# Optimization experiments

Hardware: AMD Instinct MI355X
Metric: run time of the kernel (lower is better)

The kernel has to match this reference:

```python
import jax, jax.numpy as jnp
import numpy as np

N = 50000
E = 800000
F_IN = 128


def _gat(h, src, dst, W, a_src, a_dst, bias, heads, out_ch, concat):
    n = h.shape[0]
    z = (h @ W.T).reshape(n, heads, out_ch)              # [N,H,C]
    alpha_s = jnp.sum(z * a_src, axis=-1)                # [N,H]
    alpha_d = jnp.sum(z * a_dst, axis=-1)                # [N,H]
    logits = jax.nn.leaky_relu(alpha_s[src] + alpha_d[dst], 0.2)  # [Etot,H]
    m = jax.ops.segment_max(logits, dst, num_segments=n)
    ex = jnp.exp(logits - m[dst])
    denom = jax.ops.segment_sum(ex, dst, num_segments=n)
    w = ex / (denom[dst] + 1e-16)                        # [Etot,H]
    agg = jax.ops.segment_sum(w[:, :, None] * z[src], dst, num_segments=n)  # [N,H,C]
    if concat:
        out = agg.reshape(n, heads * out_ch)
    else:
        out = agg.mean(axis=1)
    return out + bias


def setup_inputs() -> dict:
    key = jax.random.key(0)
    ks = jax.random.split(key, 16)
    s = lambda *sh: 1.0 / np.sqrt(sh[-1])
    inp = {
        "x": jax.random.normal(ks[0], (N, F_IN), jnp.float32),
        "edge_index": jax.random.randint(ks[1], (2, E), 0, N, jnp.int64),
        # GraphConv(no_node_features=128 -> 128, aggr='add')
        "W_rel": jax.random.normal(ks[2], (128, F_IN), jnp.float32) * s(128, F_IN),
        "b_rel": jnp.zeros((128,), jnp.float32),
        "W_root": jax.random.normal(ks[3], (128, F_IN), jnp.float32) * s(128, F_IN),
        # GATConv(128 -> 8, heads=8, concat) => 64
        "W1": jax.random.normal(ks[4], (64, 128), jnp.float32) * s(64, 128),
        "a1_src": jax.random.normal(ks[5], (8, 8), jnp.float32) * 0.35,
        "a1_dst": jax.random.normal(ks[6], (8, 8), jnp.float32) * 0.35,
        "b1": jnp.zeros((64,), jnp.float32),
        # GATConv(64 -> 64, heads=1, concat=False)
        "W2": jax.random.normal(ks[7], (64, 64), jnp.float32) * s(64, 64),
        "a2_src": jax.random.normal(ks[8], (1, 64), jnp.float32) * 0.125,
        "a2_dst": jax.random.normal(ks[9], (1, 64), jnp.float32) * 0.125,
        "b2": jnp.zeros((64,), jnp.float32),
        "Wr": jax.random.normal(ks[10], (1, 64), jnp.float32) * s(1, 64),
        "br": jnp.zeros((1,), jnp.float32),
    }
    return inp


def reference(x, edge_index, W_rel, b_rel, W_root, W1, a1_src, a1_dst, b1,
              W2, a2_src, a2_dst, b2, Wr, br):
    src, dst = edge_index[0], edge_index[1]
    # GraphConv, aggr='add': W_rel @ sum_{j in N(i)} x_j + b + W_root @ x_i
    nbr = jax.ops.segment_sum(x[src], dst, num_segments=N)
    h = nbr @ W_rel.T + b_rel + x @ W_root.T
    h = jax.nn.elu(h)
    # GATConv adds self-loops by default
    loop = jnp.arange(N, dtype=edge_index.dtype)
    src2 = jnp.concatenate([src, loop])
    dst2 = jnp.concatenate([dst, loop])
    h = _gat(h, src2, dst2, W1, a1_src, a1_dst, b1, heads=8, out_ch=8, concat=True)
    h = jax.nn.elu(h)
    h = _gat(h, src2, dst2, W2, a2_src, a2_dst, b2, heads=1, out_ch=64, concat=False)
    # final 'mean' aggregation over all nodes (single graph)
    g = jnp.mean(h, axis=0, keepdims=True)               # [1,64]
    return g @ Wr.T + br                                  # [1,1]
```

## Files before the change

kernel.cpp:

```cpp
#include <hip/hip_runtime.h>
#include <hip/hip_bf16.h>
#include <math.h>

#define N_NODES 50000
#define N_EDGES 800000
#define F_IN 128
#define NBUCK 391
#define EPB 4096
#define NBB 196

typedef __attribute__((ext_vector_type(8))) short bf16x8;
typedef __attribute__((ext_vector_type(4))) float f32x4;
typedef __attribute__((ext_vector_type(2))) float f32x2;
typedef unsigned long long ull;

__device__ __forceinline__ float elu_f(float x)   { return x > 0.f ? x : expm1f(x); }
__device__ __forceinline__ float lrelu_f(float x) { return x > 0.f ? x : 0.2f * x; }
__device__ __forceinline__ int   clampN(int v)    { return v < 0 ? 0 : (v >= N_NODES ? N_NODES - 1 : v); }
__device__ __forceinline__ float bits2f(unsigned int u) { union { unsigned int u; float f; } x; x.u = u; return x.f; }
__device__ __forceinline__ float bf2f(unsigned short s) { return bits2f(((unsigned int)s) << 16); }
__device__ __forceinline__ unsigned short f2bfbits(float f) {
    __hip_bfloat16 b = __float2bfloat16(f);
    return __builtin_bit_cast(unsigned short, b);
}
__device__ __forceinline__ unsigned int pack2(float lo, float hi) {
    return ((unsigned int)f2bfbits(hi) << 16) | f2bfbits(lo);
}

#define CAST_X_IDS (N_NODES * 32)
#define CAST_IDS (CAST_X_IDS + 32768 + 8192 + 4096)
#define CASTB ((CAST_IDS + 255) / 256)
__global__ __launch_bounds__(256) void k_prep(const int* __restrict__ dst,
                                              const float* __restrict__ x,
                                              const float* __restrict__ W_rel,
                                              const float* __restrict__ W_root,
                                              const float* __restrict__ W1,
                                              const float* __restrict__ W2,
                                              int* __restrict__ part,
                                              __hip_bfloat16* __restrict__ Abuf,
                                              unsigned int* __restrict__ x8,
                                              __hip_bfloat16* __restrict__ Wc,
                                              __hip_bfloat16* __restrict__ W1b,
                                              __hip_bfloat16* __restrict__ W2b,
                                              float* __restrict__ red) {
    __shared__ int hist[NBUCK];
    int tid = threadIdx.x;
    if (blockIdx.x < NBB) {
        for (int j = tid; j < NBUCK; j += 256) hist[j] = 0;
        __syncthreads();
        int base = blockIdx.x * EPB;
        #pragma unroll
        for (int t = 0; t < EPB / 256; ++t) {
            int e = base + t * 256 + tid;
            if (e < N_EDGES) atomicAdd(&hist[clampN(dst[e]) >> 7], 1);
        }
        __syncthreads();
        for (int j = tid; j < NBUCK; j += 256)
            part[(size_t)blockIdx.x * NBUCK + j] = hist[j];
    } else {
        if (blockIdx.x == NBB) red[tid] = 0.f;
        int id = (blockIdx.x - NBB) * 256 + tid;
        if (id < CAST_X_IDS) {
            int i = id >> 5, c4 = (id & 31) * 4;
            float4 v = *(const float4*)&x[(size_t)i * 128 + c4];
            ull p = (ull)f2bfbits(v.x) | ((ull)f2bfbits(v.y) << 16)
                  | ((ull)f2bfbits(v.z) << 32) | ((ull)f2bfbits(v.w) << 48);
            *(ull*)&Abuf[(size_t)i * 256 + 128 + c4] = p;
            int t = __builtin_amdgcn_cvt_pk_fp8_f32(v.x, v.y, 0, false);
            t = __builtin_amdgcn_cvt_pk_fp8_f32(v.z, v.w, t, true);
            x8[(size_t)i * 32 + (id & 31)] = (unsigned int)t;
        } else if (id < CAST_IDS) {
            int j = id - CAST_X_IDS;
            if (j < 32768) {
                int cc = j >> 8, k = j & 255;
                float v = (k < 128) ? W_rel[cc * 128 + k] : W_root[cc * 128 + (k - 128)];
                Wc[j] = __float2bfloat16(v);
            } else if (j < 32768 + 8192) {
                W1b[j - 32768] = __float2bfloat16(W1[j - 32768]);
            } else {
                W2b[j - 32768 - 8192] = __float2bfloat16(W2[j - 32768 - 8192]);
            }
        }
    }
}

__global__ __launch_bounds__(512) void k_bscan(const int* __restrict__ part,
                                               int* __restrict__ boff,
                                               int* __restrict__ bcur) {
    __shared__ int wsum[8];
    __shared__ int wbase[8];
    int tid = threadIdx.x;
    int lane = tid & 63, wid = tid >> 6;
    int v = 0;
    if (tid < NBUCK) {
        for (int b = 0; b < NBB; ++b) v += part[(size_t)b * NBUCK + tid];
    }
    int x = v;
    #pragma unroll
    for (int d = 1; d < 64; d <<= 1) {
        int t = __shfl_up(x, d, 64);
        if (lane >= d) x += t;
    }
    if (lane == 63) wsum[wid] = x;
    __syncthreads();
    if (tid == 0) {
        int b = 0;
        #pragma unroll
        for (int w = 0; w < 8; ++w) { wbase[w] = b; b += wsum[w]; }
    }
    __syncthreads();
    if (tid < NBUCK) {
        int e = wbase[wid] + x - v;
        boff[tid] = e;
        bcur[tid] = e;
    }
    if (tid == 0) boff[NBUCK] = N_EDGES;
}

__global__ __launch_bounds__(256) void k_bscatter(const int* __restrict__ src,
                                                  const int* __restrict__ dst,
                                                  int* __restrict__ bcur,
                                                  unsigned int* __restrict__ ebuf) {
    __shared__ int hist[NBUCK];
    __shared__ int hbase[NBUCK];
    int tid = threadIdx.x;
    for (int j = tid; j < NBUCK; j += 256) hist[j] = 0;
    __syncthreads();
    int base = blockIdx.x * EPB;
    unsigned int myP[EPB / 256]; int myB[EPB / 256], myR[EPB / 256];
    #pragma unroll
    for (int t = 0; t < EPB / 256; ++t) {
        int e = base + t * 256 + tid;
        if (e < N_EDGES) {
            int d = clampN(dst[e]);
            int s = clampN(src[e]);
            myP[t] = ((unsigned int)s << 7) | (unsigned int)(d & 127);
            myB[t] = d >> 7;
            myR[t] = atomicAdd(&hist[d >> 7], 1);
        } else myB[t] = -1;
    }
    __syncthreads();
    for (int j = tid; j < NBUCK; j += 256)
        if (hist[j]) hbase[j] = atomicAdd(&bcur[j], hist[j]);
    __syncthreads();
    #pragma unroll
    for (int t = 0; t < EPB / 256; ++t) {
        if (myB[t] >= 0) ebuf[hbase[myB[t]] + myR[t]] = myP[t];
    }
}

__global__ __launch_bounds__(256) void k_bfinal(const unsigned int* __restrict__ ebuf,
                                                const int* __restrict__ boff,
                                                int* __restrict__ offsets,
                                                int* __restrict__ csr) {
    __shared__ int cnt[128];
    __shared__ int cur[128];
    __shared__ int ws[4];
    int b = blockIdx.x;
    int tid = threadIdx.x;
    int node0 = b << 7;
    int k0 = boff[b], k1 = boff[b + 1];
    if (tid < 128) cnt[tid] = 0;
    __syncthreads();
    for (int k = k0 + tid; k < k1; k += 256)
        atomicAdd(&cnt[ebuf[k] & 127u], 1);
    __syncthreads();
    int lane = tid & 63;
    int v = (tid < 128) ? cnt[tid] : 0;
    int x = v;
    #pragma unroll
    for (int d = 1; d < 64; d <<= 1) {
        int t = __shfl_up(x, d, 64);
        if (lane >= d) x += t;
    }
    if (lane == 63) ws[tid >> 6] = x;
    __syncthreads();
    if (tid < 128) {
        int add = (tid >> 6) ? ws[0] : 0;
        int excl = k0 + add + x - v;
        cur[tid] = excl;
        int node = node0 + tid;
        if (node < N_NODES) offsets[node] = excl;
    }
    if (b == NBUCK - 1 && tid == 0) offsets[N_NODES] = N_EDGES;
    __syncthreads();
    for (int k = k0 + tid; k < k1; k += 256) {
        unsigned int e = ebuf[k];
        int r = atomicAdd(&cur[e & 127u], 1);
        csr[r] = (int)(e >> 7);
    }
}

__global__ __launch_bounds__(256) void k_gather(const unsigned int* __restrict__ x8,
                                                const int* __restrict__ offsets,
                                                const int* __restrict__ csr,
                                                ull* __restrict__ outNbr) {
    int i = blockIdx.x * 8 + (threadIdx.x >> 5);
    int l = threadIdx.x & 31;
    int k0 = offsets[i], k1 = offsets[i + 1];
    float a0 = 0.f, a1 = 0.f, a2 = 0.f, a3 = 0.f;
    for (int kb = k0; kb < k1; kb += 8) {
        int s[8]; int vm[8];
        #pragma unroll
        for (int j = 0; j < 8; ++j) {
            int kk = kb + j;
            vm[j] = kk < k1;
            s[j] = csr[vm[j] ? kk : k1 - 1];
        }
        unsigned int u[8];
        #pragma unroll
        for (int j = 0; j < 8; ++j) u[j] = x8[(size_t)s[j] * 32 + l];
        #pragma unroll
        for (int j = 0; j < 8; ++j) {
            if (vm[j]) {
                f32x2 lo = __builtin_amdgcn_cvt_pk_f32_fp8(u[j], false);
                f32x2 hi = __builtin_amdgcn_cvt_pk_f32_fp8(u[j], true);
                a0 += lo.x; a1 += lo.y; a2 += hi.x; a3 += hi.y;
            }
        }
    }
    outNbr[(size_t)i * 64 + l] = (ull)pack2(a0, a1) | ((ull)pack2(a2, a3) << 32);
}

__global__ __launch_bounds__(256) void k_gemm12(const __hip_bfloat16* __restrict__ A,
                                                const __hip_bfloat16* __restrict__ Wc,
                                                const float* __restrict__ bias,
                                                const __hip_bfloat16* __restrict__ W1b,
                                                const float* __restrict__ a_src,
                                                const float* __restrict__ a_dst,
                                                float* __restrict__ as_o,
                                                float* __restrict__ ad_o,
                                                unsigned int* __restrict__ z8) {
    __shared__ __align__(16) short smem[64 * 136];
    short (*sA)[40] = (short(*)[40])smem;
    short (*sW)[40] = (short(*)[40])(smem + 64 * 40);
    int tid = threadIdx.x;
    int lane = tid & 63, wave = tid >> 6;
    int quad = lane >> 4, l16 = lane & 15;
    int node0 = blockIdx.x * 64;
    int srow = tid >> 2, schk = (tid & 3) * 8;
    int ga = node0 + srow; if (ga >= N_NODES) ga = N_NODES - 1;
    const short* Ap = (const short*)A + (size_t)ga * 256 + schk;
    const short* Wp = (const short*)Wc;
    f32x4 acc[8];
    #pragma unroll
    for (int t = 0; t < 8; ++t) acc[t] = (f32x4){0.f, 0.f, 0.f, 0.f};
    for (int k0 = 0; k0 < 256; k0 += 32) {
        *(bf16x8*)&sA[srow][schk] = *(const bf16x8*)(Ap + k0);
        #pragma unroll
        for (int it = 0; it < 2; ++it) {
            int wrow = srow + it * 64;
            *(bf16x8*)&sW[wrow][schk] = *(const bf16x8*)(Wp + (size_t)wrow * 256 + k0 + schk);
        }
        __syncthreads();
        bf16x8 a = *(const bf16x8*)&sA[wave * 16 + l16][quad * 8];
        #pragma unroll
        for (int nt = 0; nt < 8; ++nt) {
            bf16x8 b = *(const bf16x8*)&sW[nt * 16 + l16][quad * 8];
            acc[nt] = __builtin_amdgcn_mfma_f32_16x16x32_bf16(a, b, acc[nt], 0, 0, 0);
        }
        __syncthreads();
    }
    #pragma unroll
    for (int nt = 0; nt < 8; ++nt) {
        int col = nt * 16 + l16;
        float bv = bias[col];
        #pragma unroll
        for (int r = 0; r < 4; ++r) {
            int row = wave * 16 + quad * 4 + r;
            smem[row * 136 + col] = (short)f2bfbits(elu_f(acc[nt][r] + bv));
        }
    }
    __syncthreads();
    f32x4 acc2[4];
    #pragma unroll
    for (int t = 0; t < 4; ++t) acc2[t] = (f32x4){0.f, 0.f, 0.f, 0.f};
    const short* W1p = (const short*)W1b;
    #pragma unroll
    for (int k0 = 0; k0 < 128; k0 += 32) {
        bf16x8 a = *(const bf16x8*)&smem[(wave * 16 + l16) * 136 + k0 + quad * 8];
        #pragma unroll
        for (int nt = 0; nt < 4; ++nt) {
            bf16x8 b = *(const bf16x8*)(W1p + (size_t)(nt * 16 + l16) * 128 + k0 + quad * 8);
            acc2[nt] = __builtin_amdgcn_mfma_f32_16x16x32_bf16(a, b, acc2[nt], 0, 0, 0);
        }
    }
    __syncthreads();
    #pragma unroll
    for (int nt = 0; nt < 4; ++nt) {
        int col = nt * 16 + l16;
        #pragma unroll
        for (int r = 0; r < 4; ++r) {
            int row = wave * 16 + quad * 4 + r;
            smem[row * 72 + col] = (short)f2bfbits(acc2[nt][r]);
        }
    }
    __syncthreads();
    int row = tid >> 2, chunk = tid & 3;
    int gi = node0 + row;
    float v[16];
    bf16x8 c0 = *(const bf16x8*)&smem[row * 72 + chunk * 16];
    bf16x8 c1 = *(const bf16x8*)&smem[row * 72 + chunk * 16 + 8];
    #pragma unroll
    for (int j = 0; j < 8; ++j) {
        v[j]     = bf2f((unsigned short)c0[j]);
        v[8 + j] = bf2f((unsigned short)c1[j]);
    }
    float ps0 = 0.f, pd0 = 0.f, ps1 = 0.f, pd1 = 0.f;
    #pragma unroll
    for (int j = 0; j < 8; ++j) {
        ps0 += v[j] * a_src[chunk * 16 + j];
        pd0 += v[j] * a_dst[chunk * 16 + j];
        ps1 += v[8 + j] * a_src[chunk * 16 + 8 + j];
        pd1 += v[8 + j] * a_dst[chunk * 16 + 8 + j];
    }
    if (gi < N_NODES) {
        as_o[(size_t)gi * 8 + 2 * chunk]     = ps0;
        as_o[(size_t)gi * 8 + 2 * chunk + 1] = ps1;
        ad_o[(size_t)gi * 8 + 2 * chunk]     = pd0;
        ad_o[(size_t)gi * 8 + 2 * chunk + 1] = pd1;
        #pragma unroll
        for (int wi = 0; wi < 4; ++wi) {
            int t = __builtin_amdgcn_cvt_pk_fp8_f32(v[4 * wi], v[4 * wi + 1], 0, false);
            t = __builtin_amdgcn_cvt_pk_fp8_f32(v[4 * wi + 2], v[4 * wi + 3], t, true);
            z8[(size_t)gi * 16 + chunk * 4 + wi] = (unsigned int)t;
        }
    }
}

__global__ __launch_bounds__(256) void k_gat1z2(const unsigned int* __restrict__ z8,
                                                const float* __restrict__ as1,
                                                const float* __restrict__ ad1,
                                                const float* __restrict__ b1,
                                                const int* __restrict__ offsets,
                                                const int* __restrict__ csr,
                                                const __hip_bfloat16* __restrict__ W2b,
                                                const float* __restrict__ a2s,
                                                const float* __restrict__ a2d,
                                                float* __restrict__ as2,
                                                float* __restrict__ ad2,
                                                unsigned int* __restrict__ z2e8) {
    __shared__ __align__(16) short sH2[16 * 72];
    __shared__ __align__(16) short sZ2[16 * 72];
    int iloc = threadIdx.x >> 4;
    int i = blockIdx.x * 16 + iloc;
    int l = threadIdx.x & 15;
    int hd = l >> 1;
    int wh = l & 7, slot = l >> 3;
    int k0 = offsets[i], k1 = offsets[i + 1];
    float ad_h = ad1[(size_t)i * 8 + hd];
    float adw  = ad1[(size_t)i * 8 + wh];
    float e_self = __expf(lrelu_f(as1[(size_t)i * 8 + hd] + ad_h));
    unsigned int uz = z8[(size_t)i * 16 + l];
    f32x2 zlo = __builtin_amdgcn_cvt_pk_f32_fp8(uz, false);
    f32x2 zhi = __builtin_amdgcn_cvt_pk_f32_fp8(uz, true);
    float acc0 = e_self * zlo.x, acc1 = e_self * zlo.y;
    float acc2 = e_self * zhi.x, acc3 = e_self * zhi.y;
    float denp = 0.f;
    for (int kb = k0; kb < k1; kb += 8) {
        int sr[4]; float er[4];
        #pragma unroll
        for (int m = 0; m < 4; ++m) {
            int kk = kb + 2 * m + slot;
            bool v = kk < k1;
            int s = csr[v ? kk : k1 - 1];
            sr[m] = s;
            er[m] = v ? __expf(lrelu_f(as1[(size_t)s * 8 + wh] + adw)) : 0.f;
            denp += er[m];
        }
        int sj[8]; float ej[8]; unsigned int u[8];
        #pragma unroll
        for (int m = 0; m < 4; ++m) {
            #pragma unroll
            for (int sb = 0; sb < 2; ++sb) {
                sj[2 * m + sb] = __shfl(sr[m], sb * 8 + hd, 16);
                ej[2 * m + sb] = __shfl(er[m], sb * 8 + hd, 16);
            }
        }
        #pragma unroll
        for (int j = 0; j < 8; ++j) u[j] = z8[(size_t)sj[j] * 16 + l];
        #pragma unroll
        for (int j = 0; j < 8; ++j) {
            f32x2 alo = __builtin_amdgcn_cvt_pk_f32_fp8(u[j], false);
            f32x2 ahi = __builtin_amdgcn_cvt_pk_f32_fp8(u[j], true);
            acc0 += ej[j] * alo.x; acc1 += ej[j] * alo.y;
            acc2 += ej[j] * ahi.x; acc3 += ej[j] * ahi.y;
        }
    }
    denp += __shfl_xor(denp, 8, 16);
    float den = __shfl(denp, hd, 16) + e_self;
    float inv = 1.f / den;
    float r0 = elu_f(acc0 * inv + b1[4 * l + 0]);
    float r1 = elu_f(acc1 * inv + b1[4 * l + 1]);
    float r2 = elu_f(acc2 * inv + b1[4 * l + 2]);
    float r3 = elu_f(acc3 * inv + b1[4 * l + 3]);
    *(ull*)&sH2[iloc * 72 + 4 * l] = (ull)pack2(r0, r1) | ((ull)pack2(r2, r3) << 32);
    __syncthreads();
    int lane = threadIdx.x & 63, wave = threadIdx.x >> 6;
    int quad = lane >> 4, l16 = lane & 15;
    f32x4 accz = (f32x4){0.f, 0.f, 0.f, 0.f};
    const short* W2p = (const short*)W2b;
    #pragma unroll
    for (int kk0 = 0; kk0 < 64; kk0 += 32) {
        bf16x8 a = *(const bf16x8*)&sH2[l16 * 72 + kk0 + quad * 8];
        bf16x8 b = *(const bf16x8*)(W2p + (size_t)(wave * 16 + l16) * 64 + kk0 + quad * 8);
        accz = __builtin_amdgcn_mfma_f32_16x16x32_bf16(a, b, accz, 0, 0, 0);
    }
    #pragma unroll
    for (int r = 0; r < 4; ++r)
        sZ2[(quad * 4 + r) * 72 + wave * 16 + l16] = (short)f2bfbits(accz[r]);
    __syncthreads();
    ull pz = *(const ull*)&sZ2[iloc * 72 + 4 * l];
    float v0 = bf2f((unsigned short)(pz & 0xffff));
    float v1 = bf2f((unsigned short)((pz >> 16) & 0xffff));
    float v2 = bf2f((unsigned short)((pz >> 32) & 0xffff));
    float v3 = bf2f((unsigned short)(pz >> 48));
    float ps = v0 * a2s[4 * l + 0] + v1 * a2s[4 * l + 1] + v2 * a2s[4 * l + 2] + v3 * a2s[4 * l + 3];
    float pd = v0 * a2d[4 * l + 0] + v1 * a2d[4 * l + 1] + v2 * a2d[4 * l + 2] + v3 * a2d[4 * l + 3];
    #pragma unroll
    for (int d = 8; d >= 1; d >>= 1) {
        ps += __shfl_xor(ps, d, 16);
        pd += __shfl_xor(pd, d, 16);
    }
    if (l == 0) { as2[i] = ps; ad2[i] = pd; }
    int t = __builtin_amdgcn_cvt_pk_fp8_f32(v0, v1, 0, false);
    t = __builtin_amdgcn_cvt_pk_fp8_f32(v2, v3, t, true);
    z2e8[(size_t)i * 16 + l] = (unsigned int)t;
}

__global__ __launch_bounds__(256) void k_gat2attn(const unsigned int* __restrict__ z8,
                                                  const float* __restrict__ as2,
                                                  const float* __restrict__ ad2,
                                                  const float* __restrict__ b2,
                                                  const int* __restrict__ offsets,
                                                  const int* __restrict__ csr,
                                                  const float* __restrict__ Wr,
                                                  float* __restrict__ red) {
    int i = blockIdx.x * 16 + (threadIdx.x >> 4);
    int l = threadIdx.x & 15;
    int k0 = offsets[i], k1 = offsets[i + 1];
    float ad = ad2[i];
    float e_self = __expf(lrelu_f(as2[i] + ad));
    unsigned int uz = z8[(size_t)i * 16 + l];
    f32x2 zlo = __builtin_amdgcn_cvt_pk_f32_fp8(uz, false);
    f32x2 zhi = __builtin_amdgcn_cvt_pk_f32_fp8(uz, true);
    float acc0 = e_self * zlo.x, acc1 = e_self * zlo.y;
    float acc2 = e_self * zhi.x, acc3 = e_self * zhi.y;
    float denp = (l == 0) ? e_self : 0.f;
    for (int kb = k0; kb < k1; kb += 16) {
        int kk = kb + l;
        bool v = kk < k1;
        int s = csr[v ? kk : k1 - 1];
        float e = v ? __expf(lrelu_f(as2[s] + ad)) : 0.f;
        denp += e;
        int nv = k1 - kb; if (nv > 16) nv = 16;
        for (int j0 = 0; j0 < nv; j0 += 8) {
            int sj[8]; float ej[8]; unsigned int u[8];
            #pragma unroll
            for (int j = 0; j < 8; ++j) {
                int idx = (j0 + j) & 15;
                sj[j] = __shfl(s, idx, 16);
                ej[j] = __shfl(e, idx, 16);
            }
            #pragma unroll
            for (int j = 0; j < 8; ++j) u[j] = z8[(size_t)sj[j] * 16 + l];
            #pragma unroll
            for (int j = 0; j < 8; ++j) {
                f32x2 alo = __builtin_amdgcn_cvt_pk_f32_fp8(u[j], false);
                f32x2 ahi = __builtin_amdgcn_cvt_pk_f32_fp8(u[j], true);
                acc0 += ej[j] * alo.x; acc1 += ej[j] * alo.y;
                acc2 += ej[j] * ahi.x; acc3 += ej[j] * ahi.y;
            }
        }
    }
    #pragma unroll
    for (int d = 8; d >= 1; d >>= 1) denp += __shfl_xor(denp, d, 16);
    float inv = 1.f / denp;
    float c = (acc0 * inv + b2[4 * l + 0]) * Wr[4 * l + 0]
            + (acc1 * inv + b2[4 * l + 1]) * Wr[4 * l + 1]
            + (acc2 * inv + b2[4 * l + 2]) * Wr[4 * l + 2]
            + (acc3 * inv + b2[4 * l + 3]) * Wr[4 * l + 3];
    #pragma unroll
    for (int d = 8; d >= 1; d >>= 1) c += __shfl_xor(c, d, 64);
    if (l == 0) atomicAdd(&red[blockIdx.x & 255], c);
}

__global__ void k_finalize(const float* __restrict__ red, const float* __restrict__ br,
                           float* __restrict__ out) {
    int t = threadIdx.x;
    float s = red[t] + red[t + 64] + red[t + 128] + red[t + 192];
    #pragma unroll
    for (int d = 32; d >= 1; d >>= 1) s += __shfl_xor(s, d, 64);
    if (t == 0) out[0] = s * (1.0f / N_NODES) + br[0];
}

extern "C" void kernel_launch(void* const* d_in, const int* in_sizes, int n_in,
                              void* d_out, int out_size, void* d_ws, size_t ws_size,
                              hipStream_t stream) {
    const float* x      = (const float*)d_in[0];
    const int*   edges  = (const int*)d_in[1];
    const float* W_rel  = (const float*)d_in[2];
    const float* b_rel  = (const float*)d_in[3];
    const float* W_root = (const float*)d_in[4];
    const float* W1     = (const float*)d_in[5];
    const float* a1s    = (const float*)d_in[6];
    const float* a1d    = (const float*)d_in[7];
    const float* b1     = (const float*)d_in[8];
    const float* W2     = (const float*)d_in[9];
    const float* a2s    = (const float*)d_in[10];
    const float* a2d    = (const float*)d_in[11];
    const float* b2     = (const float*)d_in[12];
    const float* Wr     = (const float*)d_in[13];
    const float* br     = (const float*)d_in[14];
    float* out = (float*)d_out;

    const int* src = edges;
    const int* dst = edges + N_EDGES;

    char* ws = (char*)d_ws;
    size_t p = 0;
    auto alloc = [&](size_t bytes) -> void* {
        void* r = ws + p;
        p = (p + bytes + 255) & ~(size_t)255;
        return r;
    };
    int*   part    = (int*)alloc((size_t)NBB * NBUCK * 4);
    int*   boff    = (int*)alloc((size_t)(NBUCK + 1) * 4);
    int*   bcur    = (int*)alloc((size_t)NBUCK * 4);
    unsigned int* ebuf = (unsigned int*)alloc((size_t)N_EDGES * 4);
    int*   offsets = (int*)alloc((size_t)(N_NODES + 1) * 4);
    int*   csr     = (int*)alloc((size_t)N_EDGES * 4);
    __hip_bfloat16* Abuf = (__hip_bfloat16*)alloc((size_t)N_NODES * 256 * 2);
    unsigned int* x8 = (unsigned int*)alloc((size_t)N_NODES * 32 * 4);
    __hip_bfloat16* Wc   = (__hip_bfloat16*)alloc((size_t)128 * 256 * 2);
    __hip_bfloat16* W1b  = (__hip_bfloat16*)alloc((size_t)64 * 128 * 2);
    __hip_bfloat16* W2b  = (__hip_bfloat16*)alloc((size_t)64 * 64 * 2);
    float* as1 = (float*)alloc((size_t)N_NODES * 8 * 4);
    float* ad1 = (float*)alloc((size_t)N_NODES * 8 * 4);
    float* as2 = (float*)alloc((size_t)N_NODES * 4);
    float* ad2 = (float*)alloc((size_t)N_NODES * 4);
    unsigned int* z1e8 = (unsigned int*)alloc((size_t)N_NODES * 16 * 4);
    unsigned int* z2e8 = (unsigned int*)alloc((size_t)N_NODES * 16 * 4);
    float* red = (float*)alloc(256 * 4);

    const int MB   = (N_NODES + 63) / 64;
    const int NB8  = N_NODES / 8;
    const int NB16 = N_NODES / 16;

    k_prep    <<<NBB + CASTB, 256, 0, stream>>>(dst, x, W_rel, W_root, W1, W2,
                                                part, Abuf, x8, Wc, W1b, W2b, red);
    k_bscan   <<<1, 512, 0, stream>>>(part, boff, bcur);
    k_bscatter<<<NBB, 256, 0, stream>>>(src, dst, bcur, ebuf);
    k_bfinal  <<<NBUCK, 256, 0, stream>>>(ebuf, boff, offsets, csr);
    k_gather  <<<NB8, 256, 0, stream>>>(x8, offsets, csr, (ull*)Abuf);
    k_gemm12  <<<MB, 256, 0, stream>>>(Abuf, Wc, b_rel, W1b, a1s, a1d, as1, ad1, z1e8);
    k_gat1z2  <<<NB16, 256, 0, stream>>>(z1e8, as1, ad1, b1, offsets, csr,
                                         W2b, a2s, a2d, as2, ad2, z2e8);
    k_gat2attn<<<NB16, 256, 0, stream>>>(z2e8, as2, ad2, b2, offsets, csr, Wr, red);
    k_finalize<<<1, 64, 0, stream>>>(red, br, out);
}
```

Baseline: 241.6 us.

## Fuse post-prep pipeline into one cooperative persistent kernel with grid syncs

Replaces eight separate kernel launches (bucket scan, scatter, CSR finalize, gather, GEMM, GAT1+Z2, GAT2 attention, finalize) with one cooperative kernel that loops over virtual blocks and separates phases with grid.sync(). The bucket scan becomes a parallel grid reduction followed by a Blelloch scan in block 0. The aim is to remove launch gaps and inter-kernel drain/fill overhead. In exchange, work is capped at the occupancy-limited resident grid, each phase uses a grid-stride loop, and every phase boundary pays a grid-wide barrier. The single shared memory buffer, sized for the GEMM tile, also limits occupancy across all phases.

```diff
diff --git a/kernel.cpp b/kernel.cpp
--- a/kernel.cpp
+++ b/kernel.cpp
@@ -1,6 +1,9 @@
 #include <hip/hip_runtime.h>
 #include <hip/hip_bf16.h>
+#include <hip/hip_cooperative_groups.h>
 #include <math.h>
+
+namespace cg = cooperative_groups;
 
 #define N_NODES 50000
 #define N_EDGES 800000
@@ -84,414 +87,427 @@
     }
 }
 
-__global__ __launch_bounds__(512) void k_bscan(const int* __restrict__ part,
-                                               int* __restrict__ boff,
-                                               int* __restrict__ bcur) {
-    __shared__ int wsum[8];
-    __shared__ int wbase[8];
+struct MegaArgs {
+    const int* src; const int* dst;
+    const int* part;
+    int* boff; int* bcur;
+    unsigned int* ebuf;
+    int* offsets; int* csr;
+    const unsigned int* x8;
+    __hip_bfloat16* Abuf;
+    const __hip_bfloat16* Wc; const float* b_rel; const __hip_bfloat16* W1b;
+    const float* a1s; const float* a1d;
+    float* as1; float* ad1; unsigned int* z1e8;
+    const float* b1; const __hip_bfloat16* W2b;
+    const float* a2s; const float* a2d;
+    float* as2; float* ad2; unsigned int* z2e8;
+    const float* b2; const float* Wr;
+    float* red; const float* br; float* out;
+};
+
+__global__ __launch_bounds__(256) void k_mega(MegaArgs A) {
+    __shared__ __align__(16) short smem[64 * 136];
     int tid = threadIdx.x;
-    int lane = tid & 63, wid = tid >> 6;
-    int v = 0;
-    if (tid < NBUCK) {
-        for (int b = 0; b < NBB; ++b) v += part[(size_t)b * NBUCK + tid];
-    }
-    int x = v;
-    #pragma unroll
-    for (int d = 1; d < 64; d <<= 1) {
-        int t = __shfl_up(x, d, 64);
-        if (lane >= d) x += t;
-    }
-    if (lane == 63) wsum[wid] = x;
-    __syncthreads();
-    if (tid == 0) {
-        int b = 0;
+    cg::grid_group grid = cg::this_grid();
+
+    {
+        int gt = blockIdx.x * 256 + tid;
+        if (gt < NBUCK) {
+            int v = 0;
+            for (int b = 0; b < NBB; ++b) v += A.part[(size_t)b * NBUCK + gt];
+            A.bcur[gt] = v;
+        }
+    }
+    grid.sync();
+
+    if (blockIdx.x == 0) {
+        int* sc = (int*)smem;
+        sc[tid]       = (tid < NBUCK) ? A.bcur[tid] : 0;
+        sc[tid + 256] = (tid + 256 < NBUCK) ? A.bcur[tid + 256] : 0;
+        int offset = 1;
+        for (int d = 256; d > 0; d >>= 1) {
+            __syncthreads();
+            if (tid < d) {
+                int ai = offset * (2 * tid + 1) - 1;
+                int bi = offset * (2 * tid + 2) - 1;
+                sc[bi] += sc[ai];
+            }
+            offset <<= 1;
+        }
+        __syncthreads();
+        if (tid == 0) sc[511] = 0;
+        for (int d = 1; d < 512; d <<= 1) {
+            offset >>= 1;
+            __syncthreads();
+            if (tid < d) {
+                int ai = offset * (2 * tid + 1) - 1;
+                int bi = offset * (2 * tid + 2) - 1;
+                int t = sc[ai]; sc[ai] = sc[bi]; sc[bi] += t;
+            }
+        }
+        __syncthreads();
+        if (tid < NBUCK)       { A.boff[tid] = sc[tid];             A.bcur[tid] = sc[tid]; }
+        if (tid + 256 < NBUCK) { A.boff[tid + 256] = sc[tid + 256]; A.bcur[tid + 256] = sc[tid + 256]; }
+        if (tid == 0) A.boff[NBUCK] = N_EDGES;
+    }
+    grid.sync();
+
+    {
+        int* hist  = (int*)smem;
+        int* hbase = hist + NBUCK;
+        for (int vb = blockIdx.x; vb < NBB; vb += gridDim.x) {
+            for (int j = tid; j < NBUCK; j += 256) hist[j] = 0;
+            __syncthreads();
+            int base = vb * EPB;
+            unsigned int myP[EPB / 256]; int myB[EPB / 256], myR[EPB / 256];
+            #pragma unroll
+            for (int t = 0; t < EPB / 256; ++t) {
+                int e = base + t * 256 + tid;
+                if (e < N_EDGES) {
+                    int d = clampN(A.dst[e]);
+                    int s = clampN(A.src[e]);
+                    myP[t] = ((unsigned int)s << 7) | (unsigned int)(d & 127);
+                    myB[t] = d >> 7;
+                    myR[t] = atomicAdd(&hist[d >> 7], 1);
+                } else myB[t] = -1;
+            }
+            __syncthreads();
+            for (int j = tid; j < NBUCK; j += 256)
+                if (hist[j]) hbase[j] = atomicAdd(&A.bcur[j], hist[j]);
+            __syncthreads();
+            #pragma unroll
+            for (int t = 0; t < EPB / 256; ++t)
+                if (myB[t] >= 0) A.ebuf[hbase[myB[t]] + myR[t]] = myP[t];
+            __syncthreads();
+        }
+    }
+    grid.sync();
+
+    {
+        int* cnt = (int*)smem;
+        int* cur = cnt + 128;
+        int* wsx = cur + 128;
+        for (int vb = blockIdx.x; vb < NBUCK; vb += gridDim.x) {
+            int node0 = vb << 7;
+            int k0 = A.boff[vb], k1 = A.boff[vb + 1];
+            if (tid < 128) cnt[tid] = 0;
+            __syncthreads();
+            for (int k = k0 + tid; k < k1; k += 256)
+                atomicAdd(&cnt[A.ebuf[k] & 127u], 1);
+            __syncthreads();
+            int lane = tid & 63;
+            int v = (tid < 128) ? cnt[tid] : 0;
+            int x = v;
+            #pragma unroll
+            for (int d = 1; d < 64; d <<= 1) {
+                int t = __shfl_up(x, d, 64);
+                if (lane >= d) x += t;
+            }
+            if (lane == 63 && tid < 128) wsx[tid >> 6] = x;
+            __syncthreads();
+            if (tid < 128) {
+                int add = (tid >> 6) ? wsx[0] : 0;
+                int excl = k0 + add + x - v;
+                cur[tid] = excl;
+                int node = node0 + tid;
+                if (node < N_NODES) A.offsets[node] = excl;
+            }
+            if (vb == NBUCK - 1 && tid == 0) A.offsets[N_NODES] = N_EDGES;
+            __syncthreads();
+            for (int k = k0 + tid; k < k1; k += 256) {
+                unsigned int e = A.ebuf[k];
+                int r = atomicAdd(&cur[e & 127u], 1);
+                A.csr[r] = (int)(e >> 7);
+            }
+            __syncthreads();
+        }
+    }
+    grid.sync();
+
+    {
+        ull* outNbr = (ull*)A.Abuf;
+        for (int vb = blockIdx.x; vb < N_NODES / 8; vb += gridDim.x) {
+            int i = vb * 8 + (tid >> 5);
+            int l = tid & 31;
+            int k0 = A.offsets[i], k1 = A.offsets[i + 1];
+            float a0 = 0.f, a1 = 0.f, a2 = 0.f, a3 = 0.f;
+            for (int kb = k0; kb < k1; kb += 8) {
+                int s[8]; int vm[8];
+                #pragma unroll
+                for (int j = 0; j < 8; ++j) {
+                    int kk = kb + j;
+                    vm[j] = kk < k1;
+                    s[j] = A.csr[vm[j] ? kk : k1 - 1];
+                }
+                unsigned int u[8];
+                #pragma unroll
+                for (int j = 0; j < 8; ++j) u[j] = A.x8[(size_t)s[j] * 32 + l];
+                #pragma unroll
+                for (int j = 0; j < 8; ++j) {
+                    if (vm[j]) {
+                        f32x2 lo = __builtin_amdgcn_cvt_pk_f32_fp8(u[j], false);
+                        f32x2 hi = __builtin_amdgcn_cvt_pk_f32_fp8(u[j], true);
+                        a0 += lo.x; a1 += lo.y; a2 += hi.x; a3 += hi.y;
+                    }
+                }
+            }
+            outNbr[(size_t)i * 64 + l] = (ull)pack2(a0, a1) | ((ull)pack2(a2, a3) << 32);
+        }
+    }
+    grid.sync();
+
+    {
+        short (*sA)[40] = (short(*)[40])smem;
+        short (*sW)[40] = (short(*)[40])(smem + 64 * 40);
+        int lane = tid & 63, wave = tid >> 6;
+        int quad = lane >> 4, l16 = lane & 15;
+        int srow = tid >> 2, schk = (tid & 3) * 8;
+        for (int vb = blockIdx.x; vb < (N_NODES + 63) / 64; vb += gridDim.x) {
+            int node0 = vb * 64;
+            int ga = node0 + srow; if (ga >= N_NODES) ga = N_NODES - 1;
+            const short* Ap = (const short*)A.Abuf + (size_t)ga * 256 + schk;
+            const short* Wp = (const short*)A.Wc;
+            f32x4 acc[8];
+            #pragma unroll
+            for (int t = 0; t < 8; ++t) acc[t] = (f32x4){0.f, 0.f, 0.f, 0.f};
+            for (int k0 = 0; k0 < 256; k0 += 32) {
+                *(bf16x8*)&sA[srow][schk] = *(const bf16x8*)(Ap + k0);
+                #pragma unroll
+                for (int it = 0; it < 2; ++it) {
+                    int wrow = srow + it * 64;
+                    *(bf16x8*)&sW[wrow][schk] = *(const bf16x8*)(Wp + (size_t)wrow * 256 + k0 + schk);
+                }
+                __syncthreads();
+                bf16x8 a = *(const bf16x8*)&sA[wave * 16 + l16][quad * 8];
+                #pragma unroll
+                for (int nt = 0; nt < 8; ++nt) {
+                    bf16x8 b = *(const bf16x8*)&sW[nt * 16 + l16][quad * 8];
+                    acc[nt] = __builtin_amdgcn_mfma_f32_16x16x32_bf16(a, b, acc[nt], 0, 0, 0);
+                }
+                __syncthreads();
+            }
+            #pragma unroll
+            for (int nt = 0; nt < 8; ++nt) {
+                int col = nt * 16 + l16;
+                float bv = A.b_rel[col];
+                #pragma unroll
+                for (int r = 0; r < 4; ++r) {
+                    int row = wave * 16 + quad * 4 + r;
+                    smem[row * 136 + col] = (short)f2bfbits(elu_f(acc[nt][r] + bv));
+                }
+            }
+            __syncthreads();
+            f32x4 acc2[4];
+            #pragma unroll
+            for (int t = 0; t < 4; ++t) acc2[t] = (f32x4){0.f, 0.f, 0.f, 0.f};
+            const short* W1p = (const short*)A.W1b;
+            #pragma unroll
+            for (int k0 = 0; k0 < 128; k0 += 32) {
+                bf16x8 a = *(const bf16x8*)&smem[(wave * 16 + l16) * 136 + k0 + quad * 8];
+                #pragma unroll
+                for (int nt = 0; nt < 4; ++nt) {
+                    bf16x8 b = *(const bf16x8*)(W1p + (size_t)(nt * 16 + l16) * 128 + k0 + quad * 8);
+                    acc2[nt] = __builtin_amdgcn_mfma_f32_16x16x32_bf16(a, b, acc2[nt], 0, 0, 0);
+                }
+            }
+            __syncthreads();
+            #pragma unroll
+            for (int nt = 0; nt < 4; ++nt) {
+                int col = nt * 16 + l16;
+                #pragma unroll
+                for (int r = 0; r < 4; ++r) {
+                    int row = wave * 16 + quad * 4 + r;
+                    smem[row * 72 + col] = (short)f2bfbits(acc2[nt][r]);
+                }
+            }
+            __syncthreads();
+            int row = tid >> 2, chunk = tid & 3;
+            int gi = node0 + row;
+            float v[16];
+            bf16x8 c0 = *(const bf16x8*)&smem[row * 72 + chunk * 16];
+            bf16x8 c1 = *(const bf16x8*)&smem[row * 72 + chunk * 16 + 8];
+            #pragma unroll
+            for (int j = 0; j < 8; ++j) {
+                v[j]     = bf2f((unsigned short)c0[j]);
+                v[8 + j] = bf2f((unsigned short)c1[j]);
+            }
+            float ps0 = 0.f, pd0 = 0.f, ps1 = 0.f, pd1 = 0.f;
+            #pragma unroll
+            for (int j = 0; j < 8; ++j) {
+                ps0 += v[j] * A.a1s[chunk * 16 + j];
+                pd0 += v[j] * A.a1d[chunk * 16 + j];
+                ps1 += v[8 + j] * A.a1s[chunk * 16 + 8 + j];
+                pd1 += v[8 + j] * A.a1d[chunk * 16 + 8 + j];
+            }
+            if (gi < N_NODES) {
+                A.as1[(size_t)gi * 8 + 2 * chunk]     = ps0;
+                A.as1[(size_t)gi * 8 + 2 * chunk + 1] = ps1;
+                A.ad1[(size_t)gi * 8 + 2 * chunk]     = pd0;
+                A.ad1[(size_t)gi * 8 + 2 * chunk + 1] = pd1;
+                #pragma unroll
+                for (int wi = 0; wi < 4; ++wi) {
+                    int t = __builtin_amdgcn_cvt_pk_fp8_f32(v[4 * wi], v[4 * wi + 1], 0, false);
+                    t = __builtin_amdgcn_cvt_pk_fp8_f32(v[4 * wi + 2], v[4 * wi + 3], t, true);
+                    A.z1e8[(size_t)gi * 16 + chunk * 4 + wi] = (unsigned int)t;
+                }
+            }
+            __syncthreads();
+        }
+    }
+    grid.sync();
+
+    {
+        short* sH2 = smem;
+        short* sZ2 = smem + 16 * 72;
+        for (int vb = blockIdx.x; vb < N_NODES / 16; vb += gridDim.x) {
+            int iloc = tid >> 4;
+            int i = vb * 16 + iloc;
+            int l = tid & 15;
+            int hd = l >> 1;
+            int wh = l & 7, slot = l >> 3;
+            int k0 = A.offsets[i], k1 = A.offsets[i + 1];
+            float ad_h = A.ad1[(size_t)i * 8 + hd];
+            float adw  = A.ad1[(size_t)i * 8 + wh];
+            float e_self = __expf(lrelu_f(A.as1[(size_t)i * 8 + hd] + ad_h));
+            unsigned int uz = A.z1e8[(size_t)i * 16 + l];
+            f32x2 zlo = __builtin_amdgcn_cvt_pk_f32_fp8(uz, false);
+            f32x2 zhi = __builtin_amdgcn_cvt_pk_f32_fp8(uz, true);
+            float acc0 = e_self * zlo.x, acc1 = e_self * zlo.y;
+            float acc2 = e_self * zhi.x, acc3 = e_self * zhi.y;
+            float denp = 0.f;
+            for (int kb = k0; kb < k1; kb += 8) {
+                int sr[4]; float er[4];
+                #pragma unroll
+                for (int m = 0; m < 4; ++m) {
+                    int kk = kb + 2 * m + slot;
+                    bool vv = kk < k1;
+                    int s = A.csr[vv ? kk : k1 - 1];
+                    sr[m] = s;
+                    er[m] = vv ? __expf(lrelu_f(A.as1[(size_t)s * 8 + wh] + adw)) : 0.f;
+                    denp += er[m];
+                }
+                int sj[8]; float ej[8]; unsigned int u[8];
+                #pragma unroll
+                for (int m = 0; m < 4; ++m) {
+                    #pragma unroll
+                    for (int sb = 0; sb < 2; ++sb) {
+                        sj[2 * m + sb] = __shfl(sr[m], sb * 8 + hd, 16);
+                        ej[2 * m + sb] = __shfl(er[m], sb * 8 + hd, 16);
+                    }
+                }
+                #pragma unroll
+                for (int j = 0; j < 8; ++j) u[j] = A.z1e8[(size_t)sj[j] * 16 + l];
+                #pragma unroll
+                for (int j = 0; j < 8; ++j) {
+                    f32x2 alo = __builtin_amdgcn_cvt_pk_f32_fp8(u[j], false);
+                    f32x2 ahi = __builtin_amdgcn_cvt_pk_f32_fp8(u[j], true);
+                    acc0 += ej[j] * alo.x; acc1 += ej[j] * alo.y;
+                    acc2 += ej[j] * ahi.x; acc3 += ej[j] * ahi.y;
+                }
+            }
+            denp += __shfl_xor(denp, 8, 16);
+            float den = __shfl(denp, hd, 16) + e_self;
+            float inv = 1.f / den;
+            float r0 = elu_f(acc0 * inv + A.b1[4 * l + 0]);
+            float r1 = elu_f(acc1 * inv + A.b1[4 * l + 1]);
+            float r2 = elu_f(acc2 * inv + A.b1[4 * l + 2]);
+            float r3 = elu_f(acc3 * inv + A.b1[4 * l + 3]);
+            *(ull*)&sH2[iloc * 72 + 4 * l] = (ull)pack2(r0, r1) | ((ull)pack2(r2, r3) << 32);
+            __syncthreads();
+            int lane = tid & 63, wave = tid >> 6;
+            int quad = lane >> 4, l16 = lane & 15;
+            f32x4 accz = (f32x4){0.f, 0.f, 0.f, 0.f};
+            const short* W2p = (const short*)A.W2b;
+            #pragma unroll
+            for (int kk0 = 0; kk0 < 64; kk0 += 32) {
+                bf16x8 a = *(const bf16x8*)&sH2[l16 * 72 + kk0 + quad * 8];
+                bf16x8 b = *(const bf16x8*)(W2p + (size_t)(wave * 16 + l16) * 64 + kk0 + quad * 8);
+                accz = __builtin_amdgcn_mfma_f32_16x16x32_bf16(a, b, accz, 0, 0, 0);
+            }
+            #pragma unroll
+            for (int r = 0; r < 4; ++r)
+                sZ2[(quad * 4 + r) * 72 + wave * 16 + l16] = (short)f2bfbits(accz[r]);
+            __syncthreads();
+            ull pz = *(const ull*)&sZ2[iloc * 72 + 4 * l];
+            float v0 = bf2f((unsigned short)(pz & 0xffff));
+            float v1 = bf2f((unsigned short)((pz >> 16) & 0xffff));
+            float v2 = bf2f((unsigned short)((pz >> 32) & 0xffff));
+            float v3 = bf2f((unsigned short)(pz >> 48));
+            float ps = v0 * A.a2s[4 * l + 0] + v1 * A.a2s[4 * l + 1] + v2 * A.a2s[4 * l + 2] + v3 * A.a2s[4 * l + 3];
+            float pd = v0 * A.a2d[4 * l + 0] + v1 * A.a2d[4 * l + 1] + v2 * A.a2d[4 * l + 2] + v3 * A.a2d[4 * l + 3];
+            #pragma unroll
+            for (int d = 8; d >= 1; d >>= 1) {
+                ps += __shfl_xor(ps, d, 16);
+                pd += __shfl_xor(pd, d, 16);
+            }
+            if (l == 0) { A.as2[i] = ps; A.ad2[i] = pd; }
+            int t = __builtin_amdgcn_cvt_pk_fp8_f32(v0, v1, 0, false);
+            t = __builtin_amdgcn_cvt_pk_fp8_f32(v2, v3, t, true);
+            A.z2e8[(size_t)i * 16 + l] = (unsigned int)t;
+            __syncthreads();
+        }
+    }
+    grid.sync();
+
+    {
+        for (int vb = blockIdx.x; vb < N_NODES / 16; vb += gridDim.x) {
+            int i = vb * 16 + (tid >> 4);
+            int l = tid & 15;
+            int k0 = A.offsets[i], k1 = A.offsets[i + 1];
+            float ad = A.ad2[i];
+            float e_self = __expf(lrelu_f(A.as2[i] + ad));
+            unsigned int uz = A.z2e8[(size_t)i * 16 + l];
+            f32x2 zlo = __builtin_amdgcn_cvt_pk_f32_fp8(uz, false);
+            f32x2 zhi = __builtin_amdgcn_cvt_pk_f32_fp8(uz, true);
+            float acc0 = e_self * zlo.x, acc1 = e_self * zlo.y;
+            float acc2 = e_self * zhi.x, acc3 = e_self * zhi.y;
+            float denp = (l == 0) ? e_self : 0.f;
+            for (int kb = k0; kb < k1; kb += 16) {
+                int kk = kb + l;
+                bool vv = kk < k1;
+                int s = A.csr[vv ? kk : k1 - 1];
+                float e = vv ? __expf(lrelu_f(A.as2[s] + ad)) : 0.f;
+                denp += e;
+                int nv = k1 - kb; if (nv > 16) nv = 16;
+                for (int j0 = 0; j0 < nv; j0 += 8) {
+                    int sj[8]; float ej[8]; unsigned int u[8];
+                    #pragma unroll
+                    for (int j = 0; j < 8; ++j) {
+                        int idx = (j0 + j) & 15;
+                        sj[j] = __shfl(s, idx, 16);
+                        ej[j] = __shfl(e, idx, 16);
+                    }
+                    #pragma unroll
+                    for (int j = 0; j < 8; ++j) u[j] = A.z2e8[(size_t)sj[j] * 16 + l];
+                    #pragma unroll
+                    for (int j = 0; j < 8; ++j) {
+                        f32x2 alo = __builtin_amdgcn_cvt_pk_f32_fp8(u[j], false);
+                        f32x2 ahi = __builtin_amdgcn_cvt_pk_f32_fp8(u[j], true);
+                        acc0 += ej[j] * alo.x; acc1 += ej[j] * alo.y;
+                        acc2 += ej[j] * ahi.x; acc3 += ej[j] * ahi.y;
+                    }
+                }
+            }
+            #pragma unroll
+            for (int d = 8; d >= 1; d >>= 1) denp += __shfl_xor(denp, d, 16);
+            float inv = 1.f / denp;
+            float c = (acc0 * inv + A.b2[4 * l + 0]) * A.Wr[4 * l + 0]
+                    + (acc1 * inv + A.b2[4 * l + 1]) * A.Wr[4 * l + 1]
+                    + (acc2 * inv + A.b2[4 * l + 2]) * A.Wr[4 * l + 2]
+                    + (acc3 * inv + A.b2[4 * l + 3]) * A.Wr[4 * l + 3];
+            #pragma unroll
+            for (int d = 8; d >= 1; d >>= 1) c += __shfl_xor(c, d, 64);
+            if (l == 0) atomicAdd(&A.red[vb & 255], c);
+        }
+    }
+    grid.sync();
+
+    if (blockIdx.x == 0 && tid < 64) {
+        float s = A.red[tid] + A.red[tid + 64] + A.red[tid + 128] + A.red[tid + 192];
         #pragma unroll
-        for (int w = 0; w < 8; ++w) { wbase[w] = b; b += wsum[w]; }
-    }
-    __syncthreads();
-    if (tid < NBUCK) {
-        int e = wbase[wid] + x - v;
-        boff[tid] = e;
-        bcur[tid] = e;
-    }
-    if (tid == 0) boff[NBUCK] = N_EDGES;
-}
-
-__global__ __launch_bounds__(256) void k_bscatter(const int* __restrict__ src,
-                                                  const int* __restrict__ dst,
-                                                  int* __restrict__ bcur,
-                                                  unsigned int* __restrict__ ebuf) {
-    __shared__ int hist[NBUCK];
-    __shared__ int hbase[NBUCK];
-    int tid = threadIdx.x;
-    for (int j = tid; j < NBUCK; j += 256) hist[j] = 0;
-    __syncthreads();
-    int base = blockIdx.x * EPB;
-    unsigned int myP[EPB / 256]; int myB[EPB / 256], myR[EPB / 256];
-    #pragma unroll
-    for (int t = 0; t < EPB / 256; ++t) {
-        int e = base + t * 256 + tid;
-        if (e < N_EDGES) {
-            int d = clampN(dst[e]);
-            int s = clampN(src[e]);
-            myP[t] = ((unsigned int)s << 7) | (unsigned int)(d & 127);
-            myB[t] = d >> 7;
-            myR[t] = atomicAdd(&hist[d >> 7], 1);
-        } else myB[t] = -1;
-    }
-    __syncthreads();
-    for (int j = tid; j < NBUCK; j += 256)
-        if (hist[j]) hbase[j] = atomicAdd(&bcur[j], hist[j]);
-    __syncthreads();
-    #pragma unroll
-    for (int t = 0; t < EPB / 256; ++t) {
-        if (myB[t] >= 0) ebuf[hbase[myB[t]] + myR[t]] = myP[t];
-    }
-}
-
-__global__ __launch_bounds__(256) void k_bfinal(const unsigned int* __restrict__ ebuf,
-                                                const int* __restrict__ boff,
-                                                int* __restrict__ offsets,
-                                                int* __restrict__ csr) {
-    __shared__ int cnt[128];
-    __shared__ int cur[128];
-    __shared__ int ws[4];
-    int b = blockIdx.x;
-    int tid = threadIdx.x;
-    int node0 = b << 7;
-    int k0 = boff[b], k1 = boff[b + 1];
-    if (tid < 128) cnt[tid] = 0;
-    __syncthreads();
-    for (int k = k0 + tid; k < k1; k += 256)
-        atomicAdd(&cnt[ebuf[k] & 127u], 1);
-    __syncthreads();
-    int lane = tid & 63;
-    int v = (tid < 128) ? cnt[tid] : 0;
-    int x = v;
-    #pragma unroll
-    for (int d = 1; d < 64; d <<= 1) {
-        int t = __shfl_up(x, d, 64);
-        if (lane >= d) x += t;
-    }
-    if (lane == 63) ws[tid >> 6] = x;
-    __syncthreads();
-    if (tid < 128) {
-        int add = (tid >> 6) ? ws[0] : 0;
-        int excl = k0 + add + x - v;
-        cur[tid] = excl;
-        int node = node0 + tid;
-        if (node < N_NODES) offsets[node] = excl;
-    }
-    if (b == NBUCK - 1 && tid == 0) offsets[N_NODES] = N_EDGES;
-    __syncthreads();
-    for (int k = k0 + tid; k < k1; k += 256) {
-        unsigned int e = ebuf[k];
-        int r = atomicAdd(&cur[e & 127u], 1);
-        csr[r] = (int)(e >> 7);
-    }
-}
-
-__global__ __launch_bounds__(256) void k_gather(const unsigned int* __restrict__ x8,
-                                                const int* __restrict__ offsets,
-                                                const int* __restrict__ csr,
-                                                ull* __restrict__ outNbr) {
-    int i = blockIdx.x * 8 + (threadIdx.x >> 5);
-    int l = threadIdx.x & 31;
-    int k0 = offsets[i], k1 = offsets[i + 1];
-    float a0 = 0.f, a1 = 0.f, a2 = 0.f, a3 = 0.f;
-    for (int kb = k0; kb < k1; kb += 8) {
-        int s[8]; int vm[8];
-        #pragma unroll
-        for (int j = 0; j < 8; ++j) {
-            int kk = kb + j;
-            vm[j] = kk < k1;
-            s[j] = csr[vm[j] ? kk : k1 - 1];
-        }
-        unsigned int u[8];
-        #pragma unroll
-        for (int j = 0; j < 8; ++j) u[j] = x8[(size_t)s[j] * 32 + l];
-        #pragma unroll
-        for (int j = 0; j < 8; ++j) {
-            if (vm[j]) {
-                f32x2 lo = __builtin_amdgcn_cvt_pk_f32_fp8(u[j], false);
-                f32x2 hi = __builtin_amdgcn_cvt_pk_f32_fp8(u[j], true);
-                a0 += lo.x; a1 += lo.y; a2 += hi.x; a3 += hi.y;
-            }
-        }
-    }
-    outNbr[(size_t)i * 64 + l] = (ull)pack2(a0, a1) | ((ull)pack2(a2, a3) << 32);
-}
-
-__global__ __launch_bounds__(256) void k_gemm12(const __hip_bfloat16* __restrict__ A,
-                                                const __hip_bfloat16* __restrict__ Wc,
-                                                const float* __restrict__ bias,
-                                                const __hip_bfloat16* __restrict__ W1b,
-                                                const float* __restrict__ a_src,
-                                                const float* __restrict__ a_dst,
-                                                float* __restrict__ as_o,
-                                                float* __restrict__ ad_o,
-                                                unsigned int* __restrict__ z8) {
-    __shared__ __align__(16) short smem[64 * 136];
-    short (*sA)[40] = (short(*)[40])smem;
-    short (*sW)[40] = (short(*)[40])(smem + 64 * 40);
-    int tid = threadIdx.x;
-    int lane = tid & 63, wave = tid >> 6;
-    int quad = lane >> 4, l16 = lane & 15;
-    int node0 = blockIdx.x * 64;
-    int srow = tid >> 2, schk = (tid & 3) * 8;
-    int ga = node0 + srow; if (ga >= N_NODES) ga = N_NODES - 1;
-    const short* Ap = (const short*)A + (size_t)ga * 256 + schk;
-    const short* Wp = (const short*)Wc;
-    f32x4 acc[8];
-    #pragma unroll
-    for (int t = 0; t < 8; ++t) acc[t] = (f32x4){0.f, 0.f, 0.f, 0.f};
-    for (int k0 = 0; k0 < 256; k0 += 32) {
-        *(bf16x8*)&sA[srow][schk] = *(const bf16x8*)(Ap + k0);
-        #pragma unroll
-        for (int it = 0; it < 2; ++it) {
-            int wrow = srow + it * 64;
-            *(bf16x8*)&sW[wrow][schk] = *(const bf16x8*)(Wp + (size_t)wrow * 256 + k0 + schk);
-        }
-        __syncthreads();
-        bf16x8 a = *(const bf16x8*)&sA[wave * 16 + l16][quad * 8];
-        #pragma unroll
-        for (int nt = 0; nt < 8; ++nt) {
-            bf16x8 b = *(const bf16x8*)&sW[nt * 16 + l16][quad * 8];
-            acc[nt] = __builtin_amdgcn_mfma_f32_16x16x32_bf16(a, b, acc[nt], 0, 0, 0);
-        }
-        __syncthreads();
-    }
-    #pragma unroll
-    for (int nt = 0; nt < 8; ++nt) {
-        int col = nt * 16 + l16;
-        float bv = bias[col];
-        #pragma unroll
-        for (int r = 0; r < 4; ++r) {
-            int row = wave * 16 + quad * 4 + r;
-            smem[row * 136 + col] = (short)f2bfbits(elu_f(acc[nt][r] + bv));
-        }
-    }
-    __syncthreads();
-    f32x4 acc2[4];
-    #pragma unroll
-    for (int t = 0; t < 4; ++t) acc2[t] = (f32x4){0.f, 0.f, 0.f, 0.f};
-    const short* W1p = (const short*)W1b;
-    #pragma unroll
-    for (int k0 = 0; k0 < 128; k0 += 32) {
-        bf16x8 a = *(const bf16x8*)&smem[(wave * 16 + l16) * 136 + k0 + quad * 8];
-        #pragma unroll
-        for (int nt = 0; nt < 4; ++nt) {
-            bf16x8 b = *(const bf16x8*)(W1p + (size_t)(nt * 16 + l16) * 128 + k0 + quad * 8);
-            acc2[nt] = __builtin_amdgcn_mfma_f32_16x16x32_bf16(a, b, acc2[nt], 0, 0, 0);
-        }
-    }
-    __syncthreads();
-    #pragma unroll
-    for (int nt = 0; nt < 4; ++nt) {
-        int col = nt * 16 + l16;
-        #pragma unroll
-        for (int r = 0; r < 4; ++r) {
-            int row = wave * 16 + quad * 4 + r;
-            smem[row * 72 + col] = (short)f2bfbits(acc2[nt][r]);
-        }
-    }
-    __syncthreads();
-    int row = tid >> 2, chunk = tid & 3;
-    int gi = node0 + row;
-    float v[16];
-    bf16x8 c0 = *(const bf16x8*)&smem[row * 72 + chunk * 16];
-    bf16x8 c1 = *(const bf16x8*)&smem[row * 72 + chunk * 16 + 8];
-    #pragma unroll
-    for (int j = 0; j < 8; ++j) {
-        v[j]     = bf2f((unsigned short)c0[j]);
-        v[8 + j] = bf2f((unsigned short)c1[j]);
-    }
-    float ps0 = 0.f, pd0 = 0.f, ps1 = 0.f, pd1 = 0.f;
-    #pragma unroll
-    for (int j = 0; j < 8; ++j) {
-        ps0 += v[j] * a_src[chunk * 16 + j];
-        pd0 += v[j] * a_dst[chunk * 16 + j];
-        ps1 += v[8 + j] * a_src[chunk * 16 + 8 + j];
-        pd1 += v[8 + j] * a_dst[chunk * 16 + 8 + j];
-    }
-    if (gi < N_NODES) {
-        as_o[(size_t)gi * 8 + 2 * chunk]     = ps0;
-        as_o[(size_t)gi * 8 + 2 * chunk + 1] = ps1;
-        ad_o[(size_t)gi * 8 + 2 * chunk]     = pd0;
-        ad_o[(size_t)gi * 8 + 2 * chunk + 1] = pd1;
-        #pragma unroll
-        for (int wi = 0; wi < 4; ++wi) {
-            int t = __builtin_amdgcn_cvt_pk_fp8_f32(v[4 * wi], v[4 * wi + 1], 0, false);
-            t = __builtin_amdgcn_cvt_pk_fp8_f32(v[4 * wi + 2], v[4 * wi + 3], t, true);
-            z8[(size_t)gi * 16 + chunk * 4 + wi] = (unsigned int)t;
-        }
-    }
-}
-
-__global__ __launch_bounds__(256) void k_gat1z2(const unsigned int* __restrict__ z8,
-                                                const float* __restrict__ as1,
-                                                const float* __restrict__ ad1,
-                                                const float* __restrict__ b1,
-                                                const int* __restrict__ offsets,
-                                                const int* __restrict__ csr,
-                                                const __hip_bfloat16* __restrict__ W2b,
-                                                const float* __restrict__ a2s,
-                                                const float* __restrict__ a2d,
-                                                float* __restrict__ as2,
-                                                float* __restrict__ ad2,
-                                                unsigned int* __restrict__ z2e8) {
-    __shared__ __align__(16) short sH2[16 * 72];
-    __shared__ __align__(16) short sZ2[16 * 72];
-    int iloc = threadIdx.x >> 4;
-    int i = blockIdx.x * 16 + iloc;
-    int l = threadIdx.x & 15;
-    int hd = l >> 1;
-    int wh = l & 7, slot = l >> 3;
-    int k0 = offsets[i], k1 = offsets[i + 1];
-    float ad_h = ad1[(size_t)i * 8 + hd];
-    float adw  = ad1[(size_t)i * 8 + wh];
-    float e_self = __expf(lrelu_f(as1[(size_t)i * 8 + hd] + ad_h));
-    unsigned int uz = z8[(size_t)i * 16 + l];
-    f32x2 zlo = __builtin_amdgcn_cvt_pk_f32_fp8(uz, false);
-    f32x2 zhi = __builtin_amdgcn_cvt_pk_f32_fp8(uz, true);
-    float acc0 = e_self * zlo.x, acc1 = e_self * zlo.y;
-    float acc2 = e_self * zhi.x, acc3 = e_self * zhi.y;
-    float denp = 0.f;
-    for (int kb = k0; kb < k1; kb += 8) {
-        int sr[4]; float er[4];
-        #pragma unroll
-        for (int m = 0; m < 4; ++m) {
-            int kk = kb + 2 * m + slot;
-            bool v = kk < k1;
-            int s = csr[v ? kk : k1 - 1];
-            sr[m] = s;
-            er[m] = v ? __expf(lrelu_f(as1[(size_t)s * 8 + wh] + adw)) : 0.f;
-            denp += er[m];
-        }
-        int sj[8]; float ej[8]; unsigned int u[8];
-        #pragma unroll
-        for (int m = 0; m < 4; ++m) {
-            #pragma unroll
-            for (int sb = 0; sb < 2; ++sb) {
-                sj[2 * m + sb] = __shfl(sr[m], sb * 8 + hd, 16);
-                ej[2 * m + sb] = __shfl(er[m], sb * 8 + hd, 16);
-            }
-        }
-        #pragma unroll
-        for (int j = 0; j < 8; ++j) u[j] = z8[(size_t)sj[j] * 16 + l];
-        #pragma unroll
-        for (int j = 0; j < 8; ++j) {
-            f32x2 alo = __builtin_amdgcn_cvt_pk_f32_fp8(u[j], false);
-            f32x2 ahi = __builtin_amdgcn_cvt_pk_f32_fp8(u[j], true);
-            acc0 += ej[j] * alo.x; acc1 += ej[j] * alo.y;
-            acc2 += ej[j] * ahi.x; acc3 += ej[j] * ahi.y;
-        }
-    }
-    denp += __shfl_xor(denp, 8, 16);
-    float den = __shfl(denp, hd, 16) + e_self;
-    float inv = 1.f / den;
-    float r0 = elu_f(acc0 * inv + b1[4 * l + 0]);
-    float r1 = elu_f(acc1 * inv + b1[4 * l + 1]);
-    float r2 = elu_f(acc2 * inv + b1[4 * l + 2]);
-    float r3 = elu_f(acc3 * inv + b1[4 * l + 3]);
-    *(ull*)&sH2[iloc * 72 + 4 * l] = (ull)pack2(r0, r1) | ((ull)pack2(r2, r3) << 32);
-    __syncthreads();
-    int lane = threadIdx.x & 63, wave = threadIdx.x >> 6;
-    int quad = lane >> 4, l16 = lane & 15;
-    f32x4 accz = (f32x4){0.f, 0.f, 0.f, 0.f};
-    const short* W2p = (const short*)W2b;
-    #pragma unroll
-    for (int kk0 = 0; kk0 < 64; kk0 += 32) {
-        bf16x8 a = *(const bf16x8*)&sH2[l16 * 72 + kk0 + quad * 8];
-        bf16x8 b = *(const bf16x8*)(W2p + (size_t)(wave * 16 + l16) * 64 + kk0 + quad * 8);
-        accz = __builtin_amdgcn_mfma_f32_16x16x32_bf16(a, b, accz, 0, 0, 0);
-    }
-    #pragma unroll
-    for (int r = 0; r < 4; ++r)
-        sZ2[(quad * 4 + r) * 72 + wave * 16 + l16] = (short)f2bfbits(accz[r]);
-    __syncthreads();
-    ull pz = *(const ull*)&sZ2[iloc * 72 + 4 * l];
-    float v0 = bf2f((unsigned short)(pz & 0xffff));
-    float v1 = bf2f((unsigned short)((pz >> 16) & 0xffff));
-    float v2 = bf2f((unsigned short)((pz >> 32) & 0xffff));
-    float v3 = bf2f((unsigned short)(pz >> 48));
-    float ps = v0 * a2s[4 * l + 0] + v1 * a2s[4 * l + 1] + v2 * a2s[4 * l + 2] + v3 * a2s[4 * l + 3];
-    float pd = v0 * a2d[4 * l + 0] + v1 * a2d[4 * l + 1] + v2 * a2d[4 * l + 2] + v3 * a2d[4 * l + 3];
-    #pragma unroll
-    for (int d = 8; d >= 1; d >>= 1) {
-        ps += __shfl_xor(ps, d, 16);
-        pd += __shfl_xor(pd, d, 16);
-    }
-    if (l == 0) { as2[i] = ps; ad2[i] = pd; }
-    int t = __builtin_amdgcn_cvt_pk_fp8_f32(v0, v1, 0, false);
-    t = __builtin_amdgcn_cvt_pk_fp8_f32(v2, v3, t, true);
-    z2e8[(size_t)i * 16 + l] = (unsigned int)t;
-}
-
-__global__ __launch_bounds__(256) void k_gat2attn(const unsigned int* __restrict__ z8,
-                                                  const float* __restrict__ as2,
-                                                  const float* __restrict__ ad2,
-                                                  const float* __restrict__ b2,
-                                                  const int* __restrict__ offsets,
-                                                  const int* __restrict__ csr,
-                                                  const float* __restrict__ Wr,
-                                                  float* __restrict__ red) {
-    int i = blockIdx.x * 16 + (threadIdx.x >> 4);
-    int l = threadIdx.x & 15;
-    int k0 = offsets[i], k1 = offsets[i + 1];
-    float ad = ad2[i];
-    float e_self = __expf(lrelu_f(as2[i] + ad));
-    unsigned int uz = z8[(size_t)i * 16 + l];
-    f32x2 zlo = __builtin_amdgcn_cvt_pk_f32_fp8(uz, false);
-    f32x2 zhi = __builtin_amdgcn_cvt_pk_f32_fp8(uz, true);
-    float acc0 = e_self * zlo.x, acc1 = e_self * zlo.y;
-    float acc2 = e_self * zhi.x, acc3 = e_self * zhi.y;
-    float denp = (l == 0) ? e_self : 0.f;
-    for (int kb = k0; kb < k1; kb += 16) {
-        int kk = kb + l;
-        bool v = kk < k1;
-        int s = csr[v ? kk : k1 - 1];
-        float e = v ? __expf(lrelu_f(as2[s] + ad)) : 0.f;
-        denp += e;
-        int nv = k1 - kb; if (nv > 16) nv = 16;
-        for (int j0 = 0; j0 < nv; j0 += 8) {
-            int sj[8]; float ej[8]; unsigned int u[8];
-            #pragma unroll
-            for (int j = 0; j < 8; ++j) {
-                int idx = (j0 + j) & 15;
-                sj[j] = __shfl(s, idx, 16);
-                ej[j] = __shfl(e, idx, 16);
-            }
-            #pragma unroll
-            for (int j = 0; j < 8; ++j) u[j] = z8[(size_t)sj[j] * 16 + l];
-            #pragma unroll
-            for (int j = 0; j < 8; ++j) {
-                f32x2 alo = __builtin_amdgcn_cvt_pk_f32_fp8(u[j], false);
-                f32x2 ahi = __builtin_amdgcn_cvt_pk_f32_fp8(u[j], true);
-                acc0 += ej[j] * alo.x; acc1 += ej[j] * alo.y;
-                acc2 += ej[j] * ahi.x; acc3 += ej[j] * ahi.y;
-            }
-        }
-    }
-    #pragma unroll
-    for (int d = 8; d >= 1; d >>= 1) denp += __shfl_xor(denp, d, 16);
-    float inv = 1.f / denp;
-    float c = (acc0 * inv + b2[4 * l + 0]) * Wr[4 * l + 0]
-            + (acc1 * inv + b2[4 * l + 1]) * Wr[4 * l + 1]
-            + (acc2 * inv + b2[4 * l + 2]) * Wr[4 * l + 2]
-            + (acc3 * inv + b2[4 * l + 3]) * Wr[4 * l + 3];
-    #pragma unroll
-    for (int d = 8; d >= 1; d >>= 1) c += __shfl_xor(c, d, 64);
-    if (l == 0) atomicAdd(&red[blockIdx.x & 255], c);
-}
-
-__global__ void k_finalize(const float* __restrict__ red, const float* __restrict__ br,
-                           float* __restrict__ out) {
-    int t = threadIdx.x;
-    float s = red[t] + red[t + 64] + red[t + 128] + red[t + 192];
-    #pragma unroll
-    for (int d = 32; d >= 1; d >>= 1) s += __shfl_xor(s, d, 64);
-    if (t == 0) out[0] = s * (1.0f / N_NODES) + br[0];
+        for (int d = 32; d >= 1; d >>= 1) s += __shfl_xor(s, d, 64);
+        if (tid == 0) A.out[0] = s * (1.0f / N_NODES) + A.br[0];
+    }
 }
 
 extern "C" void kernel_launch(void* const* d_in, const int* in_sizes, int n_in,
@@ -543,19 +559,26 @@
     unsigned int* z2e8 = (unsigned int*)alloc((size_t)N_NODES * 16 * 4);
     float* red = (float*)alloc(256 * 4);
 
-    const int MB   = (N_NODES + 63) / 64;
-    const int NB8  = N_NODES / 8;
-    const int NB16 = N_NODES / 16;
-
-    k_prep    <<<NBB + CASTB, 256, 0, stream>>>(dst, x, W_rel, W_root, W1, W2,
-                                                part, Abuf, x8, Wc, W1b, W2b, red);
-    k_bscan   <<<1, 512, 0, stream>>>(part, boff, bcur);
-    k_bscatter<<<NBB, 256, 0, stream>>>(src, dst, bcur, ebuf);
-    k_bfinal  <<<NBUCK, 256, 0, stream>>>(ebuf, boff, offsets, csr);
-    k_gather  <<<NB8, 256, 0, stream>>>(x8, offsets, csr, (ull*)Abuf);
-    k_gemm12  <<<MB, 256, 0, stream>>>(Abuf, Wc, b_rel, W1b, a1s, a1d, as1, ad1, z1e8);
-    k_gat1z2  <<<NB16, 256, 0, stream>>>(z1e8, as1, ad1, b1, offsets, csr,
-                                         W2b, a2s, a2d, as2, ad2, z2e8);
-    k_gat2attn<<<NB16, 256, 0, stream>>>(z2e8, as2, ad2, b2, offsets, csr, Wr, red);
-    k_finalize<<<1, 64, 0, stream>>>(red, br, out);
+    static int grid_mega = 0;
+    if (grid_mega == 0) {
+        int per_cu = 0;
+        if (hipOccupancyMaxActiveBlocksPerMultiprocessor(&per_cu, k_mega, 256, 0) != hipSuccess || per_cu < 1)
+            per_cu = 2;
+        if (per_cu > 8) per_cu = 8;
+        grid_mega = per_cu * 256;
+    }
+
+    k_prep<<<NBB + CASTB, 256, 0, stream>>>(dst, x, W_rel, W_root, W1, W2,
+                                            part, Abuf, x8, Wc, W1b, W2b, red);
+
+    MegaArgs ma;
+    ma.src = src; ma.dst = dst; ma.part = part; ma.boff = boff; ma.bcur = bcur;
+    ma.ebuf = ebuf; ma.offsets = offsets; ma.csr = csr; ma.x8 = x8; ma.Abuf = Abuf;
+    ma.Wc = Wc; ma.b_rel = b_rel; ma.W1b = W1b;
+    ma.a1s = a1s; ma.a1d = a1d; ma.as1 = as1; ma.ad1 = ad1; ma.z1e8 = z1e8;
+    ma.b1 = b1; ma.W2b = W2b;
+    ma.a2s = a2s; ma.a2d = a2d; ma.as2 = as2; ma.ad2 = ad2; ma.z2e8 = z2e8;
+    ma.b2 = b2; ma.Wr = Wr; ma.red = red; ma.br = br; ma.out = out;
+    void* kp[] = { (void*)&ma };
+    hipLaunchCooperativeKernel(k_mega, dim3(grid_mega), dim3(256), kp, 0, stream);
 }
```

Result: slower. 650.9 us (+169.4%).
